# Kernel tuning notes

Hardware: AMD Instinct MI355X
Metric: run time of the kernel (lower is better)

Reference implementation:

```python
import jax, jax.numpy as jnp
import numpy as np

B = 2048      # batch
F = 26        # number of sparse fields
C = 64        # cardinality of each field (also #lookups per field per the module's slicing quirk)
E = 64        # embedding size
D = 13        # dense features


def setup_inputs() -> dict:
    key = jax.random.key(0)
    k0, k1, k2, k3, k4, k5 = jax.random.split(key, 6)
    sparse_feat = jax.random.randint(k0, (B, F * (C + 1) - 1), 0, C, dtype=jnp.int64)
    dense_feat = jax.random.normal(k1, (B, D), dtype=jnp.float32)
    # learned params (all fields share cardinality C so tables stack cleanly)
    lin_emb = jax.random.normal(k2, (F, C, 1), dtype=jnp.float32) * 0.01   # per-field linear embeddings
    emb_tab = jax.random.normal(k3, (F, C, E), dtype=jnp.float32) * 0.01   # per-field FM embeddings
    lin_W = jax.random.normal(k4, (F + D, 1), dtype=jnp.float32) * 0.01    # fm.linear weight (in, out=1)
    lin_b = jax.random.normal(k5, (1,), dtype=jnp.float32) * 0.01          # fm.linear bias
    return {"sparse_feat": sparse_feat, "dense_feat": dense_feat,
            "lin_emb": lin_emb, "emb_tab": emb_tab, "lin_W": lin_W, "lin_b": lin_b}


def reference(sparse_feat, dense_feat, lin_emb, emb_tab, lin_W, lin_b):
    # Per-field column offsets: field i occupies cols [i*(C+1), i*(C+1)+C) of sparse_feat
    cols = jnp.arange(F)[:, None] * (C + 1) + jnp.arange(C)[None, :]  # [F, C]
    idx = sparse_feat[:, cols]                                        # [B, F, C] int indices
    f = jnp.arange(F)[None, :, None]                                  # field selector

    # linear term: per-field 1-d embedding gather, summed over the C lookups
    lin_wx = lin_emb[f, idx, 0].sum(axis=-1)                          # [B, F]
    fm_linear_in = jnp.concatenate([lin_wx, dense_feat], axis=-1)     # [B, F+D]
    fm_linear = fm_linear_in @ lin_W + lin_b                          # [B, 1]

    # pairwise FM term over all gathered embeddings ([B, F*C, E] "fields")
    w = emb_tab[f, idx]                                               # [B, F, C, E]
    x = w.reshape(w.shape[0], F * C, E)                               # [B, F*C, E]
    s = x.sum(axis=1)                                                 # [B, E]
    sq = (x * x).sum(axis=1)                                          # [B, E]
    fm_pairwise = 0.5 * jnp.sum(s * s - sq, axis=-1, keepdims=True)   # [B, 1]

    return jax.nn.sigmoid(fm_linear + fm_pairwise)
```

## Files before the change

### kernel.cpp

```cpp
#include <hip/hip_runtime.h>
#include <hip/hip_bf16.h>
#include <math.h>

#define B 2048
#define F 26
#define C 64
#define E 64
#define D 13
#define SPARSE_W (F * (C + 1) - 1)
#define K (F * C)
#define KH (K / 2)
#define MT 16
#define ROWW 836
#define PREPB F
#define FUSEB (B / MT)
#define MAGICF 0x3C96F00Du
#define AGG 25
#define DONEW 31

typedef short short8 __attribute__((ext_vector_type(8)));
typedef float f32x4  __attribute__((ext_vector_type(4)));

#define BT_OFF   0
#define TAB_OFF  ((size_t)64 * K * 2)
#define FLAG_OFF (TAB_OFF + (size_t)K * 8)
#define WS_NEED  (FLAG_OFF + 32 * 4)

__global__ __launch_bounds__(1024) void dfm_one(
    const int*   __restrict__ sparse,
    const float* __restrict__ dense,
    const float* __restrict__ lin_emb,
    const float* __restrict__ emb_tab,
    const float* __restrict__ lin_W,
    const float* __restrict__ lin_b,
    __hip_bfloat16* __restrict__ bt,
    float2* __restrict__ tab,
    unsigned int* __restrict__ flags,
    float* __restrict__ out)
{
    __shared__ union SM {
        struct {
            unsigned int cnt[MT * ROWW];
            float sbuf[2][MT][64];
            float lin[MT];
            float s2[MT];
            float sq[MT];
            int   ready;
        } f;
        struct { float tile[64][68]; } p;
    } sm;

    const int tid  = threadIdx.x;
    const int lane = tid & 63;
    const int w    = tid >> 6;
    const int bid  = blockIdx.x;

    if (bid < PREPB) {
        const int f = bid;
        const float4* src4 = (const float4*)(emb_tab + (size_t)f * 4096);
        {
            const float4 v = src4[tid];
            const int row = tid >> 4;
            const int col = (tid * 4) & 63;
            *(float4*)&sm.p.tile[row][col] = v;
        }
        __syncthreads();

        unsigned int* btw = (unsigned int*)bt;
        #pragma unroll
        for (int it = 0; it < 2; ++it) {
            const int d = tid + it * 1024;
            const int e = d >> 5;
            const int u = d & 31;
            float lo = sm.p.tile[2 * u][e];
            float hi = sm.p.tile[2 * u + 1][e];
            __hip_bfloat16 l16 = __float2bfloat16(lo);
            __hip_bfloat16 h16 = __float2bfloat16(hi);
            btw[(size_t)e * (K / 2) + f * 32 + u] =
                ((unsigned int)*(unsigned short*)&h16 << 16)
              |  (unsigned int)*(unsigned short*)&l16;
        }
        if (tid < 64) {
            float s = 0.f;
            #pragma unroll
            for (int e = 0; e < 64; ++e) {
                const float x = sm.p.tile[tid][e];
                s = fmaf(x, x, s);
            }
            const int k = f * 64 + tid;
            tab[k] = make_float2(lin_W[f] * lin_emb[k], s);
        }
        __syncthreads();
        if (tid == 0) {
            __hip_atomic_store(&flags[f], MAGICF, __ATOMIC_RELEASE,
                               __HIP_MEMORY_SCOPE_AGENT);
            if (f == AGG) {
                bool ok = false;
                while (!ok) {
                    ok = true;
                    for (int j = 0; j < AGG; ++j) {
                        const unsigned int v = __hip_atomic_load(
                            &flags[j], __ATOMIC_ACQUIRE, __HIP_MEMORY_SCOPE_AGENT);
                        ok = ok && (v == MAGICF);
                    }
                    if (!ok) __builtin_amdgcn_s_sleep(8);
                }
                __hip_atomic_store(&flags[DONEW], MAGICF, __ATOMIC_RELEASE,
                                   __HIP_MEMORY_SCOPE_AGENT);
            }
        }
        return;
    }

    const int b0 = (bid - PREPB) * MT;

    for (int i = tid; i < MT * ROWW; i += 1024) sm.f.cnt[i] = 0u;
    __syncthreads();

    {
        const int* sp = sparse + (size_t)(b0 + w) * SPARSE_W + lane;
        int idx[F];
        #pragma unroll
        for (int f = 0; f < F; ++f) idx[f] = sp[f * (C + 1)];
        #pragma unroll
        for (int f = 0; f < F; ++f) {
            const int k = f * 64 + idx[f];
            atomicAdd(&sm.f.cnt[w * ROWW + (k >> 1)], 1u << (16 * (k & 1)));
        }
    }
    __syncthreads();

    for (int i = tid; i < MT * ROWW; i += 1024) {
        const unsigned int v = sm.f.cnt[i];
        const float flo = (float)(v & 0xffffu);
        const float fhi = (float)(v >> 16);
        sm.f.cnt[i] = (__float_as_uint(fhi) & 0xffff0000u) | (__float_as_uint(flo) >> 16);
    }

    if (tid == 0) {
        while (__hip_atomic_load(&flags[DONEW], __ATOMIC_ACQUIRE,
                                 __HIP_MEMORY_SCOPE_AGENT) != MAGICF)
            __builtin_amdgcn_s_sleep(16);
        sm.f.ready = 1;
    }
    __syncthreads();

    if (w < 8) {
        const int nt = w & 3, kh = w >> 2;
        const char*  pa = (const char*)sm.f.cnt
                        + (size_t)(lane & 15) * (ROWW * 4)
                        + kh * (KH * 2) + (lane >> 4) * 16;
        const short* pb = (const short*)bt + (size_t)(nt * 16 + (lane & 15)) * K
                        + kh * KH + (lane >> 4) * 8;
        f32x4 acc = {0.f, 0.f, 0.f, 0.f};
        #pragma unroll 13
        for (int kk = 0; kk < 26; ++kk) {
            const short8 at = *(const short8*)(pa + (size_t)kk * 64);
            const short8 bv = *(const short8*)(pb + (size_t)kk * 32);
            acc = __builtin_amdgcn_mfma_f32_16x16x32_bf16(at, bv, acc, 0, 0, 0);
        }
        const int col = nt * 16 + (lane & 15);
        const int rb  = (lane >> 4) * 4;
        #pragma unroll
        for (int r = 0; r < 4; ++r)
            sm.f.sbuf[kh][rb + r][col] = acc[r];
    } else {
        const int wd = w - 8;
        const float4* t4 = (const float4*)tab;
        #pragma unroll
        for (int rr = 0; rr < 2; ++rr) {
            const int row = wd * 2 + rr;
            const unsigned int* crow = &sm.f.cnt[row * ROWW];
            float lv = 0.f, sv = 0.f;
            #pragma unroll
            for (int it = 0; it < 13; ++it) {
                const int j = lane + it * 64;
                const unsigned int dw = crow[j];
                const float lo = __uint_as_float(dw << 16);
                const float hi = __uint_as_float(dw & 0xffff0000u);
                const float4 t = t4[j];
                lv = fmaf(lo, t.x, fmaf(hi, t.z, lv));
                sv = fmaf(lo, t.y, fmaf(hi, t.w, sv));
            }
            #pragma unroll
            for (int m = 32; m >= 1; m >>= 1) {
                lv += __shfl_xor(lv, m);
                sv += __shfl_xor(sv, m);
            }
            if (lane == 0) { sm.f.lin[row] = lv; sm.f.sq[row] = sv; }
        }
    }
    __syncthreads();

    {
        const float a = sm.f.sbuf[0][w][lane] + sm.f.sbuf[1][w][lane];
        float s2v = a * a;
        #pragma unroll
        for (int m = 32; m >= 1; m >>= 1) s2v += __shfl_xor(s2v, m);
        if (lane == 0) sm.f.s2[w] = s2v;
    }
    __syncthreads();

    if (tid < MT) {
        float x = sm.f.lin[tid] + lin_b[0] + 0.5f * (sm.f.s2[tid] - sm.f.sq[tid]);
        const float* dp = dense + (size_t)(b0 + tid) * D;
        #pragma unroll
        for (int j = 0; j < D; ++j) x = fmaf(dp[j], lin_W[F + j], x);
        out[b0 + tid] = 1.f / (1.f + expf(-x));
    }
}

__global__ __launch_bounds__(256) void dfm_fallback(
    const int*   __restrict__ sparse,
    const float* __restrict__ dense,
    const float* __restrict__ lin_emb,
    const float* __restrict__ emb_tab,
    const float* __restrict__ lin_W,
    const float* __restrict__ lin_b,
    float*       __restrict__ out)
{
    const int lane = threadIdx.x & 63;
    const int wv   = threadIdx.x >> 6;
    const int b    = blockIdx.x * 4 + wv;
    if (b >= B) return;
    const int g = lane >> 4;
    const int t = lane & 15;
    const float4* emb4 = reinterpret_cast<const float4*>(emb_tab);
    float4 s  = make_float4(0.f, 0.f, 0.f, 0.f);
    float4 sq = make_float4(0.f, 0.f, 0.f, 0.f);
    float  lin = 0.f;
    const int sbase = b * SPARSE_W;
    for (int f = 0; f < F; ++f) {
        int idxreg = sparse[sbase + f * (C + 1) + lane];
        lin = fmaf(lin_W[f], lin_emb[f * C + idxreg], lin);
        const float4* rowbase = emb4 + (size_t)(f * C) * 16 + t;
        #pragma unroll
        for (int cc = 0; cc < 16; ++cc) {
            const int c   = g * 16 + cc;
            const int idx = __shfl(idxreg, c);
            float4 w = rowbase[idx * 16];
            s.x += w.x; s.y += w.y; s.z += w.z; s.w += w.w;
            sq.x = fmaf(w.x, w.x, sq.x);
            sq.y = fmaf(w.y, w.y, sq.y);
            sq.z = fmaf(w.z, w.z, sq.z);
            sq.w = fmaf(w.w, w.w, sq.w);
        }
    }
    if (lane < D) lin = fmaf(dense[b * D + lane], lin_W[F + lane], lin);
    #pragma unroll
    for (int m = 32; m >= 1; m >>= 1) lin += __shfl_xor(lin, m);
    #pragma unroll
    for (int m = 16; m <= 32; m <<= 1) {
        s.x += __shfl_xor(s.x, m); s.y += __shfl_xor(s.y, m);
        s.z += __shfl_xor(s.z, m); s.w += __shfl_xor(s.w, m);
    }
    float sql = sq.x + sq.y + sq.z + sq.w;
    #pragma unroll
    for (int m = 32; m >= 1; m >>= 1) sql += __shfl_xor(sql, m);
    float s2 = s.x * s.x + s.y * s.y + s.z * s.z + s.w * s.w;
    #pragma unroll
    for (int m = 8; m >= 1; m >>= 1) s2 += __shfl_xor(s2, m);
    if (lane == 0) {
        const float pair = 0.5f * (s2 - sql);
        const float x = lin + lin_b[0] + pair;
        out[b] = 1.f / (1.f + expf(-x));
    }
}

extern "C" void kernel_launch(void* const* d_in, const int* in_sizes, int n_in,
                              void* d_out, int out_size, void* d_ws, size_t ws_size,
                              hipStream_t stream) {
    const int*   sparse  = (const int*)  d_in[0];
    const float* dense   = (const float*)d_in[1];
    const float* lin_emb = (const float*)d_in[2];
    const float* emb_tab = (const float*)d_in[3];
    const float* lin_W   = (const float*)d_in[4];
    const float* lin_b   = (const float*)d_in[5];
    float* out = (float*)d_out;

    if (ws_size < WS_NEED) {
        dim3 grid((B + 3) / 4), block(256);
        hipLaunchKernelGGL(dfm_fallback, grid, block, 0, stream,
                           sparse, dense, lin_emb, emb_tab, lin_W, lin_b, out);
        return;
    }

    char* ws = (char*)d_ws;
    __hip_bfloat16* bt    = (__hip_bfloat16*)(ws + BT_OFF);
    float2*         tab   = (float2*)(ws + TAB_OFF);
    unsigned int*   flags = (unsigned int*)(ws + FLAG_OFF);

    hipLaunchKernelGGL(dfm_one, dim3(PREPB + FUSEB), dim3(1024), 0, stream,
                       sparse, dense, lin_emb, emb_tab, lin_W, lin_b,
                       bt, tab, flags, out);
}
```

Before: 19.09 us.

## Vectorize sparse index loads and restructure MFMA split to drop partial-sum pass

Each wave now loads its whole sparse row as contiguous int4 vectors and decodes field and column with a magic-multiply division, replacing 26 strided scalar loads per lane. The MFMA stage moves from 8 waves splitting K in half to 4 waves covering the full K. Each wave squares and reduces its accumulators in-register and atomically adds them into s2, which removes the sbuf staging and one barrier. The remaining 12 waves take the linear and squared-sum rows. The trade-off is longer serial MFMA chains per wave, extra decode ALU work and shared-memory atomics.

```diff
diff --git a/kernel.cpp b/kernel.cpp
--- a/kernel.cpp
+++ b/kernel.cpp
@@ -9,7 +9,6 @@
 #define D 13
 #define SPARSE_W (F * (C + 1) - 1)
 #define K (F * C)
-#define KH (K / 2)
 #define MT 16
 #define ROWW 836
 #define PREPB F
@@ -17,6 +16,7 @@
 #define MAGICF 0x3C96F00Du
 #define AGG 25
 #define DONEW 31
+#define TOTDW ((size_t)B * SPARSE_W)
 
 typedef short short8 __attribute__((ext_vector_type(8)));
 typedef float f32x4  __attribute__((ext_vector_type(4)));
@@ -41,7 +41,6 @@
     __shared__ union SM {
         struct {
             unsigned int cnt[MT * ROWW];
-            float sbuf[2][MT][64];
             float lin[MT];
             float s2[MT];
             float sq[MT];
@@ -115,17 +114,38 @@
     const int b0 = (bid - PREPB) * MT;
 
     for (int i = tid; i < MT * ROWW; i += 1024) sm.f.cnt[i] = 0u;
+    if (tid < MT) sm.f.s2[tid] = 0.f;
     __syncthreads();
 
     {
-        const int* sp = sparse + (size_t)(b0 + w) * SPARSE_W + lane;
-        int idx[F];
-        #pragma unroll
-        for (int f = 0; f < F; ++f) idx[f] = sp[f * (C + 1)];
-        #pragma unroll
-        for (int f = 0; f < F; ++f) {
-            const int k = f * 64 + idx[f];
-            atomicAdd(&sm.f.cnt[w * ROWW + (k >> 1)], 1u << (16 * (k & 1)));
+        const size_t rowbase = (size_t)(b0 + w) * SPARSE_W;
+        const size_t a0 = rowbase & ~(size_t)3;
+        const int lead = (int)(rowbase - a0);
+        int4 v[7];
+        #pragma unroll
+        for (int i = 0; i < 7; ++i) {
+            size_t g = a0 + (size_t)(i * 256 + lane * 4);
+            if (g > TOTDW - 4) g = TOTDW - 4;
+            v[i] = *(const int4*)(sparse + g);
+        }
+        unsigned int* myrow = &sm.f.cnt[w * ROWW];
+        #pragma unroll
+        for (int i = 0; i < 7; ++i) {
+            const int pb = i * 256 + lane * 4 - lead;
+            const int vv[4] = { v[i].x, v[i].y, v[i].z, v[i].w };
+            #pragma unroll
+            for (int j = 0; j < 4; ++j) {
+                const unsigned int p = (unsigned int)(pb + j);
+                if (p < SPARSE_W) {
+                    const unsigned int f =
+                        (unsigned int)(((unsigned long long)p * 66076420ull) >> 32);
+                    const unsigned int c = p - f * 65u;
+                    if (c < 64u) {
+                        const int k = (int)f * 64 + vv[j];
+                        atomicAdd(&myrow[k >> 1], 1u << (16 * (k & 1)));
+                    }
+                }
+            }
         }
     }
     __syncthreads();
@@ -145,31 +165,36 @@
     }
     __syncthreads();
 
-    if (w < 8) {
-        const int nt = w & 3, kh = w >> 2;
+    if (w < 4) {
+        const int nt = w;
         const char*  pa = (const char*)sm.f.cnt
-                        + (size_t)(lane & 15) * (ROWW * 4)
-                        + kh * (KH * 2) + (lane >> 4) * 16;
+                        + (size_t)(lane & 15) * (ROWW * 4) + (lane >> 4) * 16;
         const short* pb = (const short*)bt + (size_t)(nt * 16 + (lane & 15)) * K
-                        + kh * KH + (lane >> 4) * 8;
+                        + (lane >> 4) * 8;
         f32x4 acc = {0.f, 0.f, 0.f, 0.f};
         #pragma unroll 13
-        for (int kk = 0; kk < 26; ++kk) {
+        for (int kk = 0; kk < 52; ++kk) {
             const short8 at = *(const short8*)(pa + (size_t)kk * 64);
             const short8 bv = *(const short8*)(pb + (size_t)kk * 32);
             acc = __builtin_amdgcn_mfma_f32_16x16x32_bf16(at, bv, acc, 0, 0, 0);
         }
-        const int col = nt * 16 + (lane & 15);
-        const int rb  = (lane >> 4) * 4;
-        #pragma unroll
-        for (int r = 0; r < 4; ++r)
-            sm.f.sbuf[kh][rb + r][col] = acc[r];
+        #pragma unroll
+        for (int r = 0; r < 4; ++r) {
+            const int row = (lane >> 4) * 4 + r;
+            float c = acc[r] * acc[r];
+            c += __shfl_xor(c, 1);
+            c += __shfl_xor(c, 2);
+            c += __shfl_xor(c, 4);
+            c += __shfl_xor(c, 8);
+            if ((lane & 15) == 0) atomicAdd(&sm.f.s2[row], c);
+        }
     } else {
-        const int wd = w - 8;
+        const int wd = w - 4;
         const float4* t4 = (const float4*)tab;
         #pragma unroll
         for (int rr = 0; rr < 2; ++rr) {
-            const int row = wd * 2 + rr;
+            const int row = (rr == 0) ? wd : wd + 12;
+            if (rr == 1 && wd >= 4) break;
             const unsigned int* crow = &sm.f.cnt[row * ROWW];
             float lv = 0.f, sv = 0.f;
             #pragma unroll
@@ -189,15 +214,6 @@
             }
             if (lane == 0) { sm.f.lin[row] = lv; sm.f.sq[row] = sv; }
         }
-    }
-    __syncthreads();
-
-    {
-        const float a = sm.f.sbuf[0][w][lane] + sm.f.sbuf[1][w][lane];
-        float s2v = a * a;
-        #pragma unroll
-        for (int m = 32; m >= 1; m >>= 1) s2v += __shfl_xor(s2v, m);
-        if (lane == 0) sm.f.s2[w] = s2v;
     }
     __syncthreads();
 
```

Measured after the change: 19.38 us. About the same (+1.5%).
